# Performance work log

Hardware: AMD Instinct MI355X
Metric: run time of the kernel (lower is better)

The kernel has to match this reference:

```python
import jax, jax.numpy as jnp
import numpy as np

B, N, D, FF = 4096, 8, 256, 2048
EPS = 1e-5


def _layernorm(x, gamma, beta):
    mu = jnp.mean(x, axis=-1, keepdims=True)
    var = jnp.mean((x - mu) ** 2, axis=-1, keepdims=True)
    return (x - mu) * jax.lax.rsqrt(var + EPS) * gamma + beta


def _tt_product(x, w):
    # x: [b, d_in, n], w: [d_in, d_out, n]
    # h[:, :, k] = sum_i x[:, :, i] @ w[:, :, (k - i) % n]  (circular contraction)
    n = x.shape[-1]
    k = jnp.arange(n)
    idx = (k[:, None] - k[None, :]) % n          # [k, i]
    wg = w[:, :, idx]                            # [d_in, d_out, k, i]
    return jnp.einsum('bdi,doki->bok', x, wg)    # [b, d_out, n]


def setup_inputs() -> dict:
    key = jax.random.key(0)
    ks = jax.random.split(key, 12)
    xav = lambda k, shp, fi, fo: jax.random.uniform(k, shp, jnp.float32, -1.0, 1.0) * np.sqrt(6.0 / (fi + fo))
    return {
        'ent_seq': jax.random.normal(ks[0], (B, N, D), jnp.float32),
        'w_in': xav(ks[1], (D, D, N), D, D),
        'w_out': xav(ks[2], (D, D, N), D, D),
        'W1': xav(ks[3], (FF, D), D, FF),
        'bias1': jnp.zeros((FF,), jnp.float32),
        'W2': xav(ks[4], (D, FF), FF, D),
        'bias2': jnp.zeros((D,), jnp.float32),
        'gamma1': jnp.ones((D,), jnp.float32),
        'beta1': jnp.zeros((D,), jnp.float32),
        'gamma2': jnp.ones((D,), jnp.float32),
        'beta2': jnp.zeros((D,), jnp.float32),
    }


def reference(ent_seq, w_in, w_out, W1, bias1, W2, bias2, gamma1, beta1, gamma2, beta2):
    # self-attention-like block (dropout = identity in eval mode)
    xn = _layernorm(ent_seq, gamma1, beta1)          # [B, N, D]
    xp = jnp.transpose(xn, (0, 2, 1))                # [B, D, N]
    half = xp.shape[0] // 2
    h = jnp.concatenate([_tt_product(xp[:half], w_in),
                         _tt_product(xp[half:], w_out)], axis=0)
    x = ent_seq + jnp.transpose(h, (0, 2, 1))        # residual
    # FFN block
    yn = _layernorm(x, gamma2, beta2)
    ff = jax.nn.relu(yn @ W1.T + bias1) @ W2.T + bias2
    return x + ff
```

## Files before the change

### kernel.cpp

```cpp
#include <hip/hip_runtime.h>
#include <hip/hip_bf16.h>

typedef unsigned short ushort_t;
typedef __attribute__((ext_vector_type(8))) short bf16x8;
typedef __attribute__((ext_vector_type(4))) float f32x4;

#define B_SZ 4096
#define N_SZ 8
#define D_SZ 256
#define FF_SZ 2048
#define M_SZ (B_SZ * N_SZ)
#define WELEM (D_SZ * D_SZ * N_SZ)

__device__ inline float b2f(ushort_t u) {
    union { unsigned int i; float f; } t; t.i = ((unsigned int)u) << 16; return t.f;
}
__device__ inline ushort_t f2b(float f) {
    union { unsigned int i; float f; } t; t.f = f;
    unsigned int i = t.i;
    unsigned int r = (i + 0x7fffu + ((i >> 16) & 1u)) >> 16;
    return (ushort_t)r;
}

__device__ inline void gl2lds16(const ushort_t* g, ushort_t* l) {
    __builtin_amdgcn_global_load_lds((const __attribute__((address_space(1))) void*)g,
                                     (__attribute__((address_space(3))) void*)l, 16, 0, 0);
}

__global__ __launch_bounds__(256) void prep(const float* __restrict__ w_in,
                                            const float* __restrict__ w_out,
                                            const float* __restrict__ W1,
                                            const float* __restrict__ W2,
                                            ushort_t* __restrict__ bt_in,
                                            ushort_t* __restrict__ bt_out,
                                            ushort_t* __restrict__ W1b,
                                            ushort_t* __restrict__ W2b,
                                            const float* __restrict__ xin,
                                            const float* __restrict__ gam,
                                            const float* __restrict__ bet,
                                            ushort_t* __restrict__ xnout) {
    __shared__ float tile[64][65];
    const int bid = blockIdx.x;
    const int t = threadIdx.x;
    if (bid < 256) {
        const float* w = (bid < 128) ? w_in : w_out;
        ushort_t* bt = (bid < 128) ? bt_in : bt_out;
        const int id = bid & 127;
        const int d10 = (id >> 5) * 64;
        const int j0  = (id & 31) * 64;
#pragma unroll
        for (int it = 0; it < 16; ++it) {
            const int d1l = it * 4 + (t >> 6);
            const int jl = t & 63;
            tile[d1l][jl] = w[(size_t)(d10 + d1l) * 2048 + j0 + jl];
        }
        __syncthreads();
#pragma unroll
        for (int it = 0; it < 16; ++it) {
            const int jl = it * 4 + (t >> 6);
            const int d1l = t & 63;
            const int j = j0 + jl;
            bt[(size_t)(j >> 3) * 2048 + (j & 7) * 256 + d10 + d1l] = f2b(tile[d1l][jl]);
        }
    } else if (bid < 768) {
        const int id = bid - 256;
        const float* w = (id < 256) ? W1 : W2;
        ushort_t* o = (id < 256) ? W1b : W2b;
        const size_t base = (size_t)(id & 255) * 2048 + t * 8;
        const float4 a = *(const float4*)&w[base];
        const float4 b = *(const float4*)&w[base + 4];
        *(ushort4*)&o[base]     = make_ushort4(f2b(a.x), f2b(a.y), f2b(a.z), f2b(a.w));
        *(ushort4*)&o[base + 4] = make_ushort4(f2b(b.x), f2b(b.y), f2b(b.z), f2b(b.w));
    } else {
        const int wave = t >> 6;
        const int lane = t & 63;
        const size_t row = (size_t)(bid - 768) * 4 + wave;
        const float4 v = *(const float4*)&xin[row * 256 + lane * 4];
        float s = v.x + v.y + v.z + v.w;
        float q = v.x * v.x + v.y * v.y + v.z * v.z + v.w * v.w;
#pragma unroll
        for (int off = 1; off < 64; off <<= 1) {
            s += __shfl_xor(s, off, 64);
            q += __shfl_xor(q, off, 64);
        }
        const float mu = s * (1.0f / 256.0f);
        const float var = q * (1.0f / 256.0f) - mu * mu;
        const float rs = rsqrtf(var + 1e-5f);
        const float4 g = *(const float4*)&gam[lane * 4];
        const float4 b = *(const float4*)&bet[lane * 4];
        ushort4 o;
        o.x = f2b((v.x - mu) * rs * g.x + b.x);
        o.y = f2b((v.y - mu) * rs * g.y + b.y);
        o.z = f2b((v.z - mu) * rs * g.z + b.z);
        o.w = f2b((v.w - mu) * rs * g.w + b.w);
        *(ushort4*)&xnout[row * 256 + lane * 4] = o;
    }
}

__global__ __launch_bounds__(256, 2) void tt_ln2(const ushort_t* __restrict__ A,
                                                 const ushort_t* __restrict__ Bt0,
                                                 const ushort_t* __restrict__ Bt1,
                                                 const float* __restrict__ g2,
                                                 const float* __restrict__ be2,
                                                 const float* __restrict__ entf,
                                                 ushort_t* __restrict__ yn,
                                                 ushort_t* __restrict__ xb) {
    __shared__ __attribute__((aligned(16))) ushort_t As[64 * 64];
    __shared__ __attribute__((aligned(16))) ushort_t Bs[256 * 64];
    __shared__ float red_s[64 * 4];
    __shared__ float red_q[64 * 4];

    const int t = threadIdx.x;
    const int lb = ((blockIdx.x & 1) << 8) | (blockIdx.x >> 1);
    const int m0 = lb * 64;
    const int lane = t & 63;
    const int wc = t >> 6;
    const int l16 = lane & 15, quad = lane >> 4;
    const int tr = t >> 3;
    const int csw = (((t & 7) ^ (tr & 7)) << 3);

    const ushort_t* Bt = (m0 >= M_SZ / 2) ? Bt1 : Bt0;

    f32x4 acc[4][4];
#pragma unroll
    for (int i = 0; i < 4; i++)
#pragma unroll
        for (int j = 0; j < 4; j++) acc[i][j] = (f32x4)(0.0f);

#pragma unroll 1
    for (int kt = 0; kt < 32; ++kt) {
        const int kg = kt * 64;
        __syncthreads();
#pragma unroll
        for (int p = 0; p < 2; ++p) {
            const int mrow = m0 + p * 32 + tr;
            const int kcol = kg + csw;
            const int s = kcol >> 8;
            const ushort_t* gA = A + (size_t)((mrow & ~7) + (((mrow & 7) - s) & 7)) * 256 + (kcol & 255);
            gl2lds16(gA, As + p * 2048 + t * 8);
        }
#pragma unroll
        for (int p = 0; p < 8; ++p) {
            gl2lds16(Bt + (size_t)(p * 32 + tr) * 2048 + kg + csw, Bs + p * 2048 + t * 8);
        }
        __syncthreads();

#pragma unroll
        for (int kk = 0; kk < 2; ++kk) {
            const int ac = ((((kk << 2) | quad) ^ (l16 & 7)) << 3);
            bf16x8 af[4], bfv[4];
#pragma unroll
            for (int i = 0; i < 4; i++) af[i]  = *(const bf16x8*)&As[(i * 16 + l16) * 64 + ac];
#pragma unroll
            for (int j = 0; j < 4; j++) bfv[j] = *(const bf16x8*)&Bs[(wc * 64 + j * 16 + l16) * 64 + ac];
#pragma unroll
            for (int i = 0; i < 4; i++)
#pragma unroll
                for (int j = 0; j < 4; j++)
                    acc[i][j] = __builtin_amdgcn_mfma_f32_16x16x32_bf16(af[i], bfv[j], acc[i][j], 0, 0, 0);
        }
    }

    int c[4];
#pragma unroll
    for (int j = 0; j < 4; j++) c[j] = wc * 64 + j * 16 + l16;
#pragma unroll
    for (int i = 0; i < 4; i++) {
#pragma unroll
        for (int r = 0; r < 4; r++) {
            const int rl = i * 16 + quad * 4 + r;
            const size_t grow = (size_t)(m0 + rl) * 256;
            float s = 0.0f, q = 0.0f;
#pragma unroll
            for (int j = 0; j < 4; j++) {
                float v = acc[i][j][r] + entf[grow + c[j]];
                acc[i][j][r] = v;
                s += v;
                q += v * v;
            }
#pragma unroll
            for (int off = 1; off < 16; off <<= 1) {
                s += __shfl_xor(s, off, 64);
                q += __shfl_xor(q, off, 64);
            }
            if (l16 == 0) { red_s[rl * 4 + wc] = s; red_q[rl * 4 + wc] = q; }
        }
    }
    __syncthreads();
#pragma unroll
    for (int i = 0; i < 4; i++) {
#pragma unroll
        for (int r = 0; r < 4; r++) {
            const int rl = i * 16 + quad * 4 + r;
            const size_t grow = (size_t)(m0 + rl) * 256;
            const float4 ss = *(const float4*)&red_s[rl * 4];
            const float4 qq = *(const float4*)&red_q[rl * 4];
            const float S = ss.x + ss.y + ss.z + ss.w;
            const float Q = qq.x + qq.y + qq.z + qq.w;
            const float mu = S * (1.0f / 256.0f);
            const float var = Q * (1.0f / 256.0f) - mu * mu;
            const float rs = rsqrtf(var + 1e-5f);
#pragma unroll
            for (int j = 0; j < 4; j++) {
                const float v = acc[i][j][r];
                yn[grow + c[j]] = f2b((v - mu) * rs * g2[c[j]] + be2[c[j]]);
                xb[grow + c[j]] = f2b(v);
            }
        }
    }
}

#define HSTR 264
__global__ __launch_bounds__(256, 2) void ff_fused(const ushort_t* __restrict__ yn,
                                                   const ushort_t* __restrict__ W1b,
                                                   const ushort_t* __restrict__ W2b,
                                                   const float* __restrict__ bias1,
                                                   const float* __restrict__ bias2,
                                                   const ushort_t* __restrict__ xb,
                                                   float* __restrict__ out) {
    __shared__ __attribute__((aligned(16))) ushort_t As[64 * 64];
    __shared__ __attribute__((aligned(16))) ushort_t Bs[256 * 64];
    __shared__ __attribute__((aligned(16))) ushort_t Hc[64 * HSTR];

    const int t = threadIdx.x;
    const int m0 = blockIdx.x * 64;
    const int lane = t & 63;
    const int wc = t >> 6;
    const int l16 = lane & 15, quad = lane >> 4;
    const int tr = t >> 3;
    const int csw = (((t & 7) ^ (tr & 7)) << 3);

    f32x4 acc2[4][4];
#pragma unroll
    for (int i = 0; i < 4; i++)
#pragma unroll
        for (int j = 0; j < 4; j++) acc2[i][j] = (f32x4)(0.0f);

    int c4[4];
#pragma unroll
    for (int j = 0; j < 4; j++) c4[j] = wc * 64 + j * 16 + l16;

#pragma unroll 1
    for (int c = 0; c < 8; ++c) {
        f32x4 acc1[4][4];
#pragma unroll
        for (int i = 0; i < 4; i++)
#pragma unroll
            for (int j = 0; j < 4; j++) acc1[i][j] = (f32x4)(0.0f);

#pragma unroll 1
        for (int kb = 0; kb < 4; ++kb) {
            const int kg = kb * 64;
            __syncthreads();
#pragma unroll
            for (int p = 0; p < 2; ++p)
                gl2lds16(yn + (size_t)(m0 + p * 32 + tr) * 256 + kg + csw, As + p * 2048 + t * 8);
#pragma unroll
            for (int p = 0; p < 8; ++p)
                gl2lds16(W1b + (size_t)(c * 256 + p * 32 + tr) * 256 + kg + csw, Bs + p * 2048 + t * 8);
            __syncthreads();
#pragma unroll
            for (int kk = 0; kk < 2; ++kk) {
                const int ac = ((((kk << 2) | quad) ^ (l16 & 7)) << 3);
                bf16x8 af[4], bfv[4];
#pragma unroll
                for (int i = 0; i < 4; i++) af[i]  = *(const bf16x8*)&As[(i * 16 + l16) * 64 + ac];
#pragma unroll
                for (int j = 0; j < 4; j++) bfv[j] = *(const bf16x8*)&Bs[(wc * 64 + j * 16 + l16) * 64 + ac];
#pragma unroll
                for (int i = 0; i < 4; i++)
#pragma unroll
                    for (int j = 0; j < 4; j++)
                        acc1[i][j] = __builtin_amdgcn_mfma_f32_16x16x32_bf16(af[i], bfv[j], acc1[i][j], 0, 0, 0);
            }
        }

#pragma unroll
        for (int j = 0; j < 4; j++) {
            const float bb = bias1[c * 256 + c4[j]];
#pragma unroll
            for (int i = 0; i < 4; i++) {
                const int rbase = i * 16 + quad * 4;
#pragma unroll
                for (int r = 0; r < 4; r++) {
                    float v = acc1[i][j][r] + bb;
                    v = v > 0.0f ? v : 0.0f;
                    Hc[(rbase + r) * HSTR + c4[j]] = f2b(v);
                }
            }
        }

#pragma unroll 1
        for (int kb = 0; kb < 4; ++kb) {
            __syncthreads();
#pragma unroll
            for (int p = 0; p < 8; ++p)
                gl2lds16(W2b + (size_t)(p * 32 + tr) * 2048 + c * 256 + kb * 64 + csw, Bs + p * 2048 + t * 8);
            __syncthreads();
#pragma unroll
            for (int kk = 0; kk < 2; ++kk) {
                const int ank = kb * 64 + (((kk << 2) | quad) << 3);
                const int ac  = ((((kk << 2) | quad) ^ (l16 & 7)) << 3);
                bf16x8 af[4], bfv[4];
#pragma unroll
                for (int i = 0; i < 4; i++) af[i]  = *(const bf16x8*)&Hc[(i * 16 + l16) * HSTR + ank];
#pragma unroll
                for (int j = 0; j < 4; j++) bfv[j] = *(const bf16x8*)&Bs[(wc * 64 + j * 16 + l16) * 64 + ac];
#pragma unroll
                for (int i = 0; i < 4; i++)
#pragma unroll
                    for (int j = 0; j < 4; j++)
                        acc2[i][j] = __builtin_amdgcn_mfma_f32_16x16x32_bf16(af[i], bfv[j], acc2[i][j], 0, 0, 0);
            }
        }
    }

#pragma unroll
    for (int j = 0; j < 4; j++) {
        const float b2 = bias2[c4[j]];
#pragma unroll
        for (int i = 0; i < 4; i++) {
            const int rbase = m0 + i * 16 + quad * 4;
#pragma unroll
            for (int r = 0; r < 4; r++) {
                const size_t o = (size_t)(rbase + r) * 256 + c4[j];
                out[o] = acc2[i][j][r] + b2 + b2f(xb[o]);
            }
        }
    }
}

extern "C" void kernel_launch(void* const* d_in, const int* in_sizes, int n_in,
                              void* d_out, int out_size, void* d_ws, size_t ws_size,
                              hipStream_t stream) {
    const float* ent   = (const float*)d_in[0];
    const float* w_in  = (const float*)d_in[1];
    const float* w_out = (const float*)d_in[2];
    const float* W1    = (const float*)d_in[3];
    const float* bias1 = (const float*)d_in[4];
    const float* W2    = (const float*)d_in[5];
    const float* bias2 = (const float*)d_in[6];
    const float* g1    = (const float*)d_in[7];
    const float* be1   = (const float*)d_in[8];
    const float* g2    = (const float*)d_in[9];
    const float* be2   = (const float*)d_in[10];
    float* out = (float*)d_out;

    char* ws = (char*)d_ws;
    ushort_t* xn     = (ushort_t*)ws;
    ushort_t* yn     = (ushort_t*)(ws + 16777216);
    ushort_t* xb     = (ushort_t*)(ws + 2 * 16777216);
    ushort_t* bt_in  = (ushort_t*)(ws + 3 * 16777216);
    ushort_t* bt_out = bt_in + WELEM;
    ushort_t* W1b    = bt_out + WELEM;
    ushort_t* W2b    = W1b + WELEM;

    prep<<<dim3(8960), dim3(256), 0, stream>>>(w_in, w_out, W1, W2,
                                               bt_in, bt_out, W1b, W2b,
                                               ent, g1, be1, xn);
    tt_ln2<<<dim3(M_SZ / 64), dim3(256), 0, stream>>>(xn, bt_in, bt_out, g2, be2, ent, yn, xb);
    ff_fused<<<dim3(M_SZ / 64), dim3(256), 0, stream>>>(yn, W1b, W2b, bias1, bias2, xb, out);
}
```

Baseline: 241.7 us.

## Fuse circular TT product with LN2 and FFN into a single kernel

Merges the tt_ln2 and ff_fused kernels into one kernel, tt_ff. Each block first computes its 64-row TT product, residual and LayerNorm, then runs the FFN on the same rows. This removes one kernel launch and the tail/drain gap between the two grids, and the yn/xb intermediates the block just wrote are likely still in cache when it reads them back. The cost is a larger LDS footprint per block, since the tt tiles, the Hc buffer and the reduction arrays now live in the same kernel, which could limit occupancy. The kernel also relies on intra-block visibility of the global yn/xb writes before they are re-read.

```diff
diff --git a/kernel.cpp b/kernel.cpp
--- a/kernel.cpp
+++ b/kernel.cpp
@@ -97,16 +97,23 @@
     }
 }
 
-__global__ __launch_bounds__(256, 2) void tt_ln2(const ushort_t* __restrict__ A,
-                                                 const ushort_t* __restrict__ Bt0,
-                                                 const ushort_t* __restrict__ Bt1,
-                                                 const float* __restrict__ g2,
-                                                 const float* __restrict__ be2,
-                                                 const float* __restrict__ entf,
-                                                 ushort_t* __restrict__ yn,
-                                                 ushort_t* __restrict__ xb) {
+#define HSTR 264
+__global__ __launch_bounds__(256, 2) void tt_ff(const ushort_t* __restrict__ A,
+                                                const ushort_t* __restrict__ Bt0,
+                                                const ushort_t* __restrict__ Bt1,
+                                                const float* __restrict__ g2,
+                                                const float* __restrict__ be2,
+                                                const float* __restrict__ entf,
+                                                const ushort_t* __restrict__ W1b,
+                                                const ushort_t* __restrict__ W2b,
+                                                const float* __restrict__ bias1,
+                                                const float* __restrict__ bias2,
+                                                ushort_t* __restrict__ yn,
+                                                ushort_t* __restrict__ xb,
+                                                float* __restrict__ out) {
     __shared__ __attribute__((aligned(16))) ushort_t As[64 * 64];
     __shared__ __attribute__((aligned(16))) ushort_t Bs[256 * 64];
+    __shared__ __attribute__((aligned(16))) ushort_t Hc[64 * HSTR];
     __shared__ float red_s[64 * 4];
     __shared__ float red_q[64 * 4];
 
@@ -119,126 +126,104 @@
     const int tr = t >> 3;
     const int csw = (((t & 7) ^ (tr & 7)) << 3);
 
-    const ushort_t* Bt = (m0 >= M_SZ / 2) ? Bt1 : Bt0;
-
-    f32x4 acc[4][4];
+    int c4[4];
+#pragma unroll
+    for (int j = 0; j < 4; j++) c4[j] = wc * 64 + j * 16 + l16;
+
+    {
+        const ushort_t* Bt = (m0 >= M_SZ / 2) ? Bt1 : Bt0;
+
+        f32x4 acc[4][4];
+#pragma unroll
+        for (int i = 0; i < 4; i++)
+#pragma unroll
+            for (int j = 0; j < 4; j++) acc[i][j] = (f32x4)(0.0f);
+
+#pragma unroll 1
+        for (int kt = 0; kt < 32; ++kt) {
+            const int kg = kt * 64;
+            __syncthreads();
+#pragma unroll
+            for (int p = 0; p < 2; ++p) {
+                const int mrow = m0 + p * 32 + tr;
+                const int kcol = kg + csw;
+                const int s = kcol >> 8;
+                const ushort_t* gA = A + (size_t)((mrow & ~7) + (((mrow & 7) - s) & 7)) * 256 + (kcol & 255);
+                gl2lds16(gA, As + p * 2048 + t * 8);
+            }
+#pragma unroll
+            for (int p = 0; p < 8; ++p) {
+                gl2lds16(Bt + (size_t)(p * 32 + tr) * 2048 + kg + csw, Bs + p * 2048 + t * 8);
+            }
+            __syncthreads();
+
+#pragma unroll
+            for (int kk = 0; kk < 2; ++kk) {
+                const int ac = ((((kk << 2) | quad) ^ (l16 & 7)) << 3);
+                bf16x8 af[4], bfv[4];
+#pragma unroll
+                for (int i = 0; i < 4; i++) af[i]  = *(const bf16x8*)&As[(i * 16 + l16) * 64 + ac];
+#pragma unroll
+                for (int j = 0; j < 4; j++) bfv[j] = *(const bf16x8*)&Bs[(wc * 64 + j * 16 + l16) * 64 + ac];
+#pragma unroll
+                for (int i = 0; i < 4; i++)
+#pragma unroll
+                    for (int j = 0; j < 4; j++)
+                        acc[i][j] = __builtin_amdgcn_mfma_f32_16x16x32_bf16(af[i], bfv[j], acc[i][j], 0, 0, 0);
+            }
+        }
+
+#pragma unroll
+        for (int i = 0; i < 4; i++) {
+#pragma unroll
+            for (int r = 0; r < 4; r++) {
+                const int rl = i * 16 + quad * 4 + r;
+                const size_t grow = (size_t)(m0 + rl) * 256;
+                float s = 0.0f, q = 0.0f;
+#pragma unroll
+                for (int j = 0; j < 4; j++) {
+                    float v = acc[i][j][r] + entf[grow + c4[j]];
+                    acc[i][j][r] = v;
+                    s += v;
+                    q += v * v;
+                }
+#pragma unroll
+                for (int off = 1; off < 16; off <<= 1) {
+                    s += __shfl_xor(s, off, 64);
+                    q += __shfl_xor(q, off, 64);
+                }
+                if (l16 == 0) { red_s[rl * 4 + wc] = s; red_q[rl * 4 + wc] = q; }
+            }
+        }
+        __syncthreads();
+#pragma unroll
+        for (int i = 0; i < 4; i++) {
+#pragma unroll
+            for (int r = 0; r < 4; r++) {
+                const int rl = i * 16 + quad * 4 + r;
+                const size_t grow = (size_t)(m0 + rl) * 256;
+                const float4 ss = *(const float4*)&red_s[rl * 4];
+                const float4 qq = *(const float4*)&red_q[rl * 4];
+                const float S = ss.x + ss.y + ss.z + ss.w;
+                const float Q = qq.x + qq.y + qq.z + qq.w;
+                const float mu = S * (1.0f / 256.0f);
+                const float var = Q * (1.0f / 256.0f) - mu * mu;
+                const float rs = rsqrtf(var + 1e-5f);
+#pragma unroll
+                for (int j = 0; j < 4; j++) {
+                    const float v = acc[i][j][r];
+                    yn[grow + c4[j]] = f2b((v - mu) * rs * g2[c4[j]] + be2[c4[j]]);
+                    xb[grow + c4[j]] = f2b(v);
+                }
+            }
+        }
+    }
+
+    f32x4 acc2[4][4];
 #pragma unroll
     for (int i = 0; i < 4; i++)
 #pragma unroll
-        for (int j = 0; j < 4; j++) acc[i][j] = (f32x4)(0.0f);
-
-#pragma unroll 1
-    for (int kt = 0; kt < 32; ++kt) {
-        const int kg = kt * 64;
-        __syncthreads();
-#pragma unroll
-        for (int p = 0; p < 2; ++p) {
-            const int mrow = m0 + p * 32 + tr;
-            const int kcol = kg + csw;
-            const int s = kcol >> 8;
-            const ushort_t* gA = A + (size_t)((mrow & ~7) + (((mrow & 7) - s) & 7)) * 256 + (kcol & 255);
-            gl2lds16(gA, As + p * 2048 + t * 8);
-        }
-#pragma unroll
-        for (int p = 0; p < 8; ++p) {
-            gl2lds16(Bt + (size_t)(p * 32 + tr) * 2048 + kg + csw, Bs + p * 2048 + t * 8);
-        }
-        __syncthreads();
-
-#pragma unroll
-        for (int kk = 0; kk < 2; ++kk) {
-            const int ac = ((((kk << 2) | quad) ^ (l16 & 7)) << 3);
-            bf16x8 af[4], bfv[4];
-#pragma unroll
-            for (int i = 0; i < 4; i++) af[i]  = *(const bf16x8*)&As[(i * 16 + l16) * 64 + ac];
-#pragma unroll
-            for (int j = 0; j < 4; j++) bfv[j] = *(const bf16x8*)&Bs[(wc * 64 + j * 16 + l16) * 64 + ac];
-#pragma unroll
-            for (int i = 0; i < 4; i++)
-#pragma unroll
-                for (int j = 0; j < 4; j++)
-                    acc[i][j] = __builtin_amdgcn_mfma_f32_16x16x32_bf16(af[i], bfv[j], acc[i][j], 0, 0, 0);
-        }
-    }
-
-    int c[4];
-#pragma unroll
-    for (int j = 0; j < 4; j++) c[j] = wc * 64 + j * 16 + l16;
-#pragma unroll
-    for (int i = 0; i < 4; i++) {
-#pragma unroll
-        for (int r = 0; r < 4; r++) {
-            const int rl = i * 16 + quad * 4 + r;
-            const size_t grow = (size_t)(m0 + rl) * 256;
-            float s = 0.0f, q = 0.0f;
-#pragma unroll
-            for (int j = 0; j < 4; j++) {
-                float v = acc[i][j][r] + entf[grow + c[j]];
-                acc[i][j][r] = v;
-                s += v;
-                q += v * v;
-            }
-#pragma unroll
-            for (int off = 1; off < 16; off <<= 1) {
-                s += __shfl_xor(s, off, 64);
-                q += __shfl_xor(q, off, 64);
-            }
-            if (l16 == 0) { red_s[rl * 4 + wc] = s; red_q[rl * 4 + wc] = q; }
-        }
-    }
-    __syncthreads();
-#pragma unroll
-    for (int i = 0; i < 4; i++) {
-#pragma unroll
-        for (int r = 0; r < 4; r++) {
-            const int rl = i * 16 + quad * 4 + r;
-            const size_t grow = (size_t)(m0 + rl) * 256;
-            const float4 ss = *(const float4*)&red_s[rl * 4];
-            const float4 qq = *(const float4*)&red_q[rl * 4];
-            const float S = ss.x + ss.y + ss.z + ss.w;
-            const float Q = qq.x + qq.y + qq.z + qq.w;
-            const float mu = S * (1.0f / 256.0f);
-            const float var = Q * (1.0f / 256.0f) - mu * mu;
-            const float rs = rsqrtf(var + 1e-5f);
-#pragma unroll
-            for (int j = 0; j < 4; j++) {
-                const float v = acc[i][j][r];
-                yn[grow + c[j]] = f2b((v - mu) * rs * g2[c[j]] + be2[c[j]]);
-                xb[grow + c[j]] = f2b(v);
-            }
-        }
-    }
-}
-
-#define HSTR 264
-__global__ __launch_bounds__(256, 2) void ff_fused(const ushort_t* __restrict__ yn,
-                                                   const ushort_t* __restrict__ W1b,
-                                                   const ushort_t* __restrict__ W2b,
-                                                   const float* __restrict__ bias1,
-                                                   const float* __restrict__ bias2,
-                                                   const ushort_t* __restrict__ xb,
-                                                   float* __restrict__ out) {
-    __shared__ __attribute__((aligned(16))) ushort_t As[64 * 64];
-    __shared__ __attribute__((aligned(16))) ushort_t Bs[256 * 64];
-    __shared__ __attribute__((aligned(16))) ushort_t Hc[64 * HSTR];
-
-    const int t = threadIdx.x;
-    const int m0 = blockIdx.x * 64;
-    const int lane = t & 63;
-    const int wc = t >> 6;
-    const int l16 = lane & 15, quad = lane >> 4;
-    const int tr = t >> 3;
-    const int csw = (((t & 7) ^ (tr & 7)) << 3);
-
-    f32x4 acc2[4][4];
-#pragma unroll
-    for (int i = 0; i < 4; i++)
-#pragma unroll
         for (int j = 0; j < 4; j++) acc2[i][j] = (f32x4)(0.0f);
-
-    int c4[4];
-#pragma unroll
-    for (int j = 0; j < 4; j++) c4[j] = wc * 64 + j * 16 + l16;
 
 #pragma unroll 1
     for (int c = 0; c < 8; ++c) {
@@ -358,6 +343,7 @@
     prep<<<dim3(8960), dim3(256), 0, stream>>>(w_in, w_out, W1, W2,
                                                bt_in, bt_out, W1b, W2b,
                                                ent, g1, be1, xn);
-    tt_ln2<<<dim3(M_SZ / 64), dim3(256), 0, stream>>>(xn, bt_in, bt_out, g2, be2, ent, yn, xb);
-    ff_fused<<<dim3(M_SZ / 64), dim3(256), 0, stream>>>(yn, W1b, W2b, bias1, bias2, xb, out);
-}
+    tt_ff<<<dim3(M_SZ / 64), dim3(256), 0, stream>>>(xn, bt_in, bt_out, g2, be2, ent,
+                                                     W1b, W2b, bias1, bias2,
+                                                     yn, xb, out);
+}
```

Result: faster. 234.6 us (-2.9%).
